# Optimization experiments

Hardware: AMD Instinct MI355X
Metric: run time of the kernel (lower is better)

Reference implementation:

```python
import jax, jax.numpy as jnp
import numpy as np

NEG_SLOPE = 0.2   # LeakyReLU default negative slope (GATv2 + nn.LeakyReLU)
K_NEIGH = 16      # att_args['num_neighs']


def leaky(x):
    return jnp.where(x >= 0, x, NEG_SLOPE * x)


def knn_idx(x_feat, y_feat, k):
    """Per-batch KNN of y in x (feature space). x_feat,y_feat: [B,M,C] -> [B,M,k] local idx into x."""
    d = (jnp.sum(y_feat * y_feat, -1, keepdims=True)
         - 2.0 * jnp.einsum('bmc,bnc->bmn', y_feat, x_feat)
         + jnp.sum(x_feat * x_feat, -1)[:, None, :])   # [B,M,M]
    _, idx = jax.lax.top_k(-d, k)
    return idx


def gatv2_bipartite(x_last, x_past, nbr, Wl, Wr, att_w):
    """Faithful GATv2Conv((last, past), edge_index) with flow='target_to_source',
    heads H, concat=False (mean over heads), bias=False, no self loops.
    x_j = lin_l(x[0]=last) gathered at knn neighbor (col) indices,
    x_i = lin_r(x[1]=past) at query (row) indices; each query has exactly K edges."""
    N, C = x_last.shape
    H = att_w.shape[0]
    xl = (x_last @ Wl).reshape(N, H, C)          # [N,H,C]
    xr = (x_past @ Wr).reshape(N, H, C)          # [N,H,C]
    xlj = xl[nbr]                                 # [N,K,H,C] gathered source msgs
    e = jnp.einsum('nkhc,hc->nkh', leaky(xlj + xr[:, None]), att_w)  # [N,K,H]
    a = jax.nn.softmax(e, axis=1)                 # softmax over each target's K edges
    out = jnp.einsum('nkh,nkhc->nhc', a, xlj)     # [N,H,C]
    return out.mean(axis=1)                       # concat=False -> head mean, [N,C]


def reference(pc_encoded_seq, W1, b1, W2, b2, Wl, Wr, att_w, batch_size, m_points):
    T, N, C = pc_encoded_seq.shape
    B, M = batch_size, m_points
    G = W2.shape[1]
    # node_level_proj (Linear-LeakyReLU-Linear-LeakyReLU) + global_mean_pool per frame
    h = leaky(leaky(pc_encoded_seq @ W1 + b1) @ W2 + b2)      # [T,N,G]
    global_fea = h.reshape(T, B, M, G).mean(axis=2)            # [T,B,G]
    # frame-level ScaledDotProductAttention: q = last frame, k=v = past frames
    q = global_fea[-1][:, None, :]                             # [B,1,G]
    kv = jnp.transpose(global_fea[:-1], (1, 0, 2))             # [B,T-1,G]
    score = jnp.einsum('bqg,btg->bqt', q, kv) / jnp.sqrt(jnp.asarray(G, jnp.float32))
    attn = jax.nn.softmax(score, axis=-1)                      # [B,1,T-1]
    last = pc_encoded_seq[-1]                                  # [N,C]
    lastb = last.reshape(B, M, C)
    offs = (jnp.arange(B) * M)[:, None, None]
    res = []
    for i in range(T - 1):   # small fixed frame count
        past = pc_encoded_seq[i]
        nbr = knn_idx(past.reshape(B, M, C), lastb, K_NEIGH) + offs  # global idx
        out = gatv2_bipartite(last, past, nbr.reshape(N, K_NEIGH), Wl, Wr, att_w)
        res.append(out.reshape(B, M, C))
    res = jnp.stack(res, axis=1)                               # [B,T-1,M,C]
    fw = attn[:, 0, :, None, None]                             # [B,T-1,1,1]
    weighted = jnp.sum(res * fw, axis=1)                       # [B,M,C]
    tm_out = jnp.concatenate([last, weighted.reshape(N, C)], axis=-1)  # [N,2C]
    return tm_out


def setup_inputs() -> dict:
    key = jax.random.key(0)
    ks = jax.random.split(key, 8)
    T, B, M, C, G, H = 5, 4, 4096, 128, 1024, 4
    N = B * M
    s = lambda fan: 1.0 / np.sqrt(fan)
    return {
        'pc_encoded_seq': jax.random.normal(ks[0], (T, N, C), jnp.float32),
        'W1': jax.random.normal(ks[1], (C, 128), jnp.float32) * s(C),
        'b1': jnp.zeros((128,), jnp.float32),
        'W2': jax.random.normal(ks[2], (128, G), jnp.float32) * s(128),
        'b2': jnp.zeros((G,), jnp.float32),
        'Wl': jax.random.normal(ks[3], (C, H * C), jnp.float32) * s(C),
        'Wr': jax.random.normal(ks[4], (C, H * C), jnp.float32) * s(C),
        'att_w': jax.random.normal(ks[5], (H, C), jnp.float32) * s(C),
        'batch_size': B,
        'm_points': M,
    }
```

## Files before the change

### kernel.cpp

```cpp
#include <hip/hip_runtime.h>
#include <hip/hip_bf16.h>
#include <hip/hip_fp16.h>


typedef __bf16 v8bf __attribute__((ext_vector_type(8)));
typedef float  v4f  __attribute__((ext_vector_type(4)));

__device__ __forceinline__ float lrelu(float x) { return fmaxf(x, 0.2f * x); }

__device__ __forceinline__ unsigned short f2bf(float x) {
  __hip_bfloat16 h = __float2bfloat16(x);
  return __builtin_bit_cast(unsigned short, h);
}
__device__ __forceinline__ float bf2f(unsigned short u) {
  unsigned int t = ((unsigned int)u) << 16;
  return __builtin_bit_cast(float, t);
}

__device__ __forceinline__ unsigned fkey(float v) {
  unsigned b = __builtin_bit_cast(unsigned, v);
  return b ^ (((unsigned)((int)b >> 31)) | 0x80000000u);
}
__device__ __forceinline__ float finv(unsigned k) {
  unsigned m = (unsigned)((int)k >> 31);
  unsigned b = k ^ ((~m) | 0x80000000u);
  return __builtin_bit_cast(float, b);
}

#define GLOAD_LDS16(gp, lp)                                                   \
  __builtin_amdgcn_global_load_lds(                                           \
      (const __attribute__((address_space(1))) void*)(gp),                    \
      (__attribute__((address_space(3))) void*)(lp), 16, 0, 0)

#define RBAR() do { __builtin_amdgcn_s_barrier(); asm volatile("" ::: "memory"); } while (0)
#define LWAIT() do { asm volatile("s_waitcnt lgkmcnt(0)" ::: "memory");        \
                     __builtin_amdgcn_sched_barrier(0); } while (0)

template<int EP>
__global__ __launch_bounds__(256, 2)
void nt_mfma(const unsigned short* __restrict__ A, const unsigned short* __restrict__ B,
             const float* __restrict__ aux, void* __restrict__ outv, int K, int ldc)
{
  __shared__ __align__(16) unsigned short smem[3 * 8192];
  const int tid = threadIdx.x;
  const int l = tid & 63;
  const int w = tid >> 6;
  const int wm = w & 1, wn = w >> 1;
  const int m0 = blockIdx.y << 7, n0 = blockIdx.x << 7;
  const int fr = l & 15, quad = l >> 4;
  const int kt = K >> 5;
  const int xq4 = quad ^ ((fr >> 1) & 3);

  const int r0 = tid >> 2;
  const int sw = (tid & 3) ^ ((tid >> 3) & 3);
  const unsigned short* Aa = A + (size_t)(m0 + r0) * K + sw * 8;
  const unsigned short* Ab = Aa + (size_t)64 * K;
  const unsigned short* Ba = B + (size_t)(n0 + r0) * K + sw * 8;
  const unsigned short* Bb = Ba + (size_t)64 * K;

  auto stage = [&](int bi, int ks) {
    unsigned short* As = smem + bi * 8192;
    unsigned short* Bs = As + 4096;
    GLOAD_LDS16(Aa + ks * 32, As + tid * 8);
    GLOAD_LDS16(Ab + ks * 32, As + (tid + 256) * 8);
    GLOAD_LDS16(Ba + ks * 32, Bs + tid * 8);
    GLOAD_LDS16(Bb + ks * 32, Bs + (tid + 256) * 8);
  };

  v4f acc[4][4];
#pragma unroll
  for (int i = 0; i < 4; ++i)
#pragma unroll
    for (int j = 0; j < 4; ++j) acc[i][j] = (v4f){0.f, 0.f, 0.f, 0.f};

  stage(0, 0);
  if (kt > 1) stage(1, 1);
  int cur = 0, pend = (kt > 1) ? 2 : 1, sn = 2;

  for (int ks = 0; ks < kt; ++ks) {
    if (pend == 2) asm volatile("s_waitcnt vmcnt(4)" ::: "memory");
    else           asm volatile("s_waitcnt vmcnt(0)" ::: "memory");
    RBAR();
    int nb = cur + 2; if (nb >= 3) nb -= 3;
    if (sn < kt) { stage(nb, sn); ++sn; } else { --pend; }
    const unsigned short* As = smem + cur * 8192;
    const unsigned short* Bs = As + 4096;
    v8bf af[4], bfr[4];
#pragma unroll
    for (int i = 0; i < 4; ++i)
      af[i] = *(const v8bf*)(As + (wm * 64 + i * 16 + fr) * 32 + xq4 * 8);
#pragma unroll
    for (int j = 0; j < 4; ++j)
      bfr[j] = *(const v8bf*)(Bs + (wn * 64 + j * 16 + fr) * 32 + xq4 * 8);
#pragma unroll
    for (int i = 0; i < 4; ++i)
#pragma unroll
      for (int j = 0; j < 4; ++j)
        acc[i][j] = __builtin_amdgcn_mfma_f32_16x16x32_bf16(af[i], bfr[j], acc[i][j], 0, 0, 0);
    __builtin_amdgcn_sched_barrier(0);
    if (++cur == 3) cur = 0;
  }

  if (EP == 1) {
    unsigned short* O = (unsigned short*)outv;
#pragma unroll
    for (int j = 0; j < 4; ++j) {
      int col = n0 + wn * 64 + j * 16 + fr;
      float bias = aux[col];
#pragma unroll
      for (int i = 0; i < 4; ++i) {
        int row = m0 + wm * 64 + i * 16 + quad * 4;
#pragma unroll
        for (int r = 0; r < 4; ++r)
          O[(size_t)(row + r) * ldc + col] = f2bf(lrelu(acc[i][j][r] + bias));
      }
    }
  } else if (EP == 2) {
    __syncthreads();
    float* red = (float*)smem;
#pragma unroll
    for (int j = 0; j < 4; ++j) {
      int lcol = wn * 64 + j * 16 + fr;
      float bias = aux[n0 + lcol];
      float s = 0.f;
#pragma unroll
      for (int i = 0; i < 4; ++i)
#pragma unroll
        for (int r = 0; r < 4; ++r) s += lrelu(acc[i][j][r] + bias);
      s += __shfl_xor(s, 16);
      s += __shfl_xor(s, 32);
      if (quad == 0) red[w * 128 + lcol] = s;
    }
    __syncthreads();
    if (tid < 128) {
      float s = (tid < 64) ? red[0 * 128 + tid] + red[1 * 128 + tid]
                           : red[2 * 128 + tid] + red[3 * 128 + tid];
      atomicAdd((float*)outv + ((m0 >> 12) << 10) + n0 + tid, s * (1.0f / 4096.0f));
    }
  } else {
    __half* O = (__half*)outv;
#pragma unroll
    for (int j = 0; j < 4; ++j) {
      int col = n0 + wn * 64 + j * 16 + fr;
#pragma unroll
      for (int i = 0; i < 4; ++i) {
        int row = m0 + wm * 64 + i * 16 + quad * 4;
#pragma unroll
        for (int r = 0; r < 4; ++r)
          O[(size_t)(row + r) * ldc + col] = __float2half(acc[i][j][r]);
      }
    }
  }
}

#define TOPN 20
#define FB   10
#define PSTR 11

__global__ __launch_bounds__(256, 4)
void knn_coarse(const unsigned short* __restrict__ seqbf,
                const float* __restrict__ xsq, int* __restrict__ candOut)
{
  __shared__ __align__(16) unsigned short bsm[8192];
  __shared__ unsigned pushK[64 * PSTR];
  __shared__ int      cntW[64];

  const int tid = threadIdx.x;
  const int l = tid & 63;
  const int w = tid >> 6;
  const int blk = blockIdx.x;
  const int pair = ((blk & 7) << 1) | ((blk >> 3) & 1);
  const int rb = blk >> 4;
  const int f = pair >> 2, b = pair & 3;
  const int m0 = rb << 6;
  const int fr = l & 15, quad = l >> 4;
  const int xq4 = quad ^ ((fr >> 1) & 3);

  const unsigned short* ybase = seqbf + ((size_t)65536 + b * 4096) * 128;
  const unsigned short* xbase = seqbf + ((size_t)(f * 16384 + b * 4096)) * 128;
  const float* xq = xsq + f * 16384 + b * 4096;

  const int r0 = tid >> 2;
  const int sw = (tid & 3) ^ ((tid >> 3) & 3);

  v8bf afr[4];
#pragma unroll
  for (int ksp = 0; ksp < 4; ++ksp)
    afr[ksp] = *(const v8bf*)(ybase + (size_t)(m0 + w * 16 + fr) * 128 + ksp * 32 + quad * 8);

  unsigned tk[TOPN];
#pragma unroll
  for (int k = 0; k < TOPN; ++k) tk[k] = 0u;
  float tauReg = -3.0e38f;
  if (l < 16) cntW[w * 16 + l] = 0;
  float tc[4];
#pragma unroll
  for (int r = 0; r < 4; ++r) tc[r] = -3.0e38f;
  LWAIT();

  for (int ct = 0; ct < 32; ++ct) {
    const int n0 = ct << 7;
    const unsigned short* Bt = xbase + (size_t)(n0 + r0) * 128 + sw * 8;

    RBAR();
    GLOAD_LDS16(Bt, bsm + tid * 8);
    GLOAD_LDS16(Bt + 64 * 128, bsm + (tid + 256) * 8);
    GLOAD_LDS16(Bt + 32, bsm + 4096 + tid * 8);
    GLOAD_LDS16(Bt + 64 * 128 + 32, bsm + 4096 + (tid + 256) * 8);
    float xsv[8];
#pragma unroll
    for (int j = 0; j < 8; ++j) xsv[j] = xq[n0 + j * 16 + fr];
    asm volatile("s_waitcnt vmcnt(0)" ::: "memory");
    RBAR();

    v4f acc[8];
#pragma unroll
    for (int j = 0; j < 8; ++j) acc[j] = (v4f){0.f, 0.f, 0.f, 0.f};

#pragma unroll
    for (int ksp = 0; ksp < 2; ++ksp) {
      v8bf bfr[8];
#pragma unroll
      for (int j = 0; j < 8; ++j)
        bfr[j] = *(const v8bf*)(bsm + ksp * 4096 + (j * 16 + fr) * 32 + xq4 * 8);
#pragma unroll
      for (int j = 0; j < 8; ++j)
        acc[j] = __builtin_amdgcn_mfma_f32_16x16x32_bf16(afr[ksp], bfr[j], acc[j], 0, 0, 0);
    }
    LWAIT();
    RBAR();

    GLOAD_LDS16(Bt + 2 * 32, bsm + tid * 8);
    GLOAD_LDS16(Bt + 64 * 128 + 2 * 32, bsm + (tid + 256) * 8);
    GLOAD_LDS16(Bt + 3 * 32, bsm + 4096 + tid * 8);
    GLOAD_LDS16(Bt + 64 * 128 + 3 * 32, bsm + 4096 + (tid + 256) * 8);
    asm volatile("s_waitcnt vmcnt(0)" ::: "memory");
    RBAR();

#pragma unroll
    for (int ksp = 0; ksp < 2; ++ksp) {
      v8bf bfr[8];
#pragma unroll
      for (int j = 0; j < 8; ++j)
        bfr[j] = *(const v8bf*)(bsm + ksp * 4096 + (j * 16 + fr) * 32 + xq4 * 8);
#pragma unroll
      for (int j = 0; j < 8; ++j)
        acc[j] = __builtin_amdgcn_mfma_f32_16x16x32_bf16(afr[2 + ksp], bfr[j], acc[j], 0, 0, 0);
    }

#pragma unroll
    for (int j = 0; j < 8; ++j)
#pragma unroll
      for (int r = 0; r < 4; ++r)
        acc[j][r] = 2.f * acc[j][r] - xsv[j];

    if (ct == 0) {
#pragma unroll
      for (int r = 0; r < 4; ++r) {
        float t1 = fmaxf(acc[0][r], acc[1][r]);
        float t2 = fminf(acc[0][r], acc[1][r]);
#pragma unroll
        for (int j = 2; j < 8; ++j) {
          float v = acc[j][r];
          float hi = fmaxf(t1, v);
          t2 = fmaxf(t2, fminf(t1, v));
          t1 = hi;
        }
#pragma unroll
        for (int off = 1; off <= 8; off <<= 1)
          t2 = fminf(t2, __shfl_xor(t2, off));
        tc[r] = t2;
        float tq = __shfl(t2, (l >> 2) << 4);
        if (l < 16 && (l & 3) == r) tauReg = tq;
      }
    }

    unsigned int pushed = 0u;
    for (;;) {
#pragma unroll
      for (int r = 0; r < 4; ++r) {
        const float tau = tc[r];
        int mca = 0;
#pragma unroll
        for (int j = 0; j < 8; ++j) {
          const int bit = j * 4 + r;
          if (acc[j][r] >= tau && !((pushed >> bit) & 1u)) mca |= (1 << j);
        }
        if (__any(mca != 0)) {
          const int lrow = w * 16 + quad * 4 + r;
#pragma unroll
          for (int j = 0; j < 8; ++j)
            if ((mca >> j) & 1) {
              int pos = atomicAdd(&cntW[lrow], 1);
              if (pos < FB) {
                pushK[lrow * PSTR + pos] =
                    (fkey(acc[j][r]) & 0xFFFFF000u) | (unsigned)(n0 + j * 16 + fr);
                pushed |= (1u << (j * 4 + r));
              }
            }
        }
      }
      LWAIT();
      bool ov = false;
      if (l < 16) {
        const int grow = w * 16 + l;
        int c = cntW[grow];
        int cc = c < FB ? c : FB;
        for (int q = 0; q < cc; ++q) {
          unsigned k = pushK[grow * PSTR + q];
          if (k > tk[TOPN - 1]) {
#pragma unroll
            for (int i = TOPN - 1; i >= 1; --i)
              tk[i] = (k > tk[i - 1]) ? tk[i - 1] : (k > tk[i] ? k : tk[i]);
            tk[0] = (k > tk[0]) ? k : tk[0];
          }
        }
        if (tk[TOPN - 1] != 0u)
          tauReg = fmaxf(tauReg, finv(tk[TOPN - 1] & 0xFFFFF000u));
        ov = c > FB;
        cntW[grow] = 0;
      }
      LWAIT();
#pragma unroll
      for (int r = 0; r < 4; ++r)
        tc[r] = __shfl(tauReg, quad * 4 + r);
      if (!__any(ov)) break;
    }
  }

  if (l < 16) {
    const int grow = w * 16 + l;
    int* outp = candOut + ((size_t)(f * 16384 + b * 4096 + m0 + grow)) * TOPN;
#pragma unroll
    for (int k = 0; k < TOPN; ++k) outp[k] = (int)(tk[k] & 0xFFFu);
  }
}

__global__ __launch_bounds__(256)
void knn_rescore(const float* __restrict__ seq, const float* __restrict__ xsq,
                 const int* __restrict__ cand, int* __restrict__ nbrOut)
{
  __shared__ float sc[4][20];
  const int tid = threadIdx.x;
  const int l = tid & 63;
  const int wq = tid >> 6;
  const int blk = blockIdx.x;
  const int pair = ((blk & 7) << 1) | ((blk >> 3) & 1);
  const int qb = blk >> 4;
  const int f = pair >> 2, b = pair & 3;
  const int qloc = qb * 4 + wq;
  const int gq = pair * 4096 + qloc;

  const int c8 = l & 7;
  const int h  = l >> 3;
  const float* yrow = seq + ((size_t)65536 + b * 4096 + qloc) * 128 + h * 16;
  float4 y0 = *(const float4*)(yrow);
  float4 y1 = *(const float4*)(yrow + 4);
  float4 y2 = *(const float4*)(yrow + 8);
  float4 y3 = *(const float4*)(yrow + 12);
  const float* xslice = seq + (size_t)(f * 16384 + (b << 12)) * 128;
  const float* xsqs = xsq + f * 16384 + (b << 12);
  const int* cq = cand + (size_t)gq * 20;

#pragma unroll
  for (int rd = 0; rd < 3; ++rd) {
    int cr = rd * 8 + c8;
    int crc = cr < 20 ? cr : 0;
    int cj = cq[crc];
    const float* xr = xslice + (size_t)cj * 128 + h * 16;
    float4 x0 = *(const float4*)(xr);
    float4 x1 = *(const float4*)(xr + 4);
    float4 x2 = *(const float4*)(xr + 8);
    float4 x3 = *(const float4*)(xr + 12);
    float p = y0.x * x0.x + y0.y * x0.y + y0.z * x0.z + y0.w * x0.w
            + y1.x * x1.x + y1.y * x1.y + y1.z * x1.z + y1.w * x1.w
            + y2.x * x2.x + y2.y * x2.y + y2.z * x2.z + y2.w * x2.w
            + y3.x * x3.x + y3.y * x3.y + y3.z * x3.z + y3.w * x3.w;
    p += __shfl_xor(p, 8);
    p += __shfl_xor(p, 16);
    p += __shfl_xor(p, 32);
    if (h == 0 && cr < 20) sc[wq][cr] = 2.f * p - xsqs[cj];
  }
  LWAIT();
  if (l < 20) {
    float myv = sc[wq][l];
    int rank = 0;
#pragma unroll
    for (int j = 0; j < 20; ++j) {
      float vj = sc[wq][j];
      rank += (vj > myv || (vj == myv && j < l)) ? 1 : 0;
    }
    if (rank < 16)
      nbrOut[(size_t)gq * 16 + rank] = (b << 12) + cq[l];
  }
}

__global__ __launch_bounds__(256)
void convert_inputs(const float* __restrict__ seq, unsigned short* __restrict__ seqbf,
                    unsigned short* __restrict__ ylay, unsigned short* __restrict__ xlay,
                    float* __restrict__ xsq)
{
  const int tid = threadIdx.x;
  const int row = blockIdx.x * 8 + (tid >> 5);
  const int c4 = tid & 31;
  float4 v = *(const float4*)(seq + (size_t)row * 128 + c4 * 4);
  ushort4 hi, lo;
  hi.x = f2bf(v.x); lo.x = f2bf(v.x - bf2f(hi.x));
  hi.y = f2bf(v.y); lo.y = f2bf(v.y - bf2f(hi.y));
  hi.z = f2bf(v.z); lo.z = f2bf(v.z - bf2f(hi.z));
  hi.w = f2bf(v.w); lo.w = f2bf(v.w - bf2f(hi.w));
  *(ushort4*)(seqbf + (size_t)row * 128 + c4 * 4) = hi;
  float ss = v.x * v.x + v.y * v.y + v.z * v.z + v.w * v.w;
#pragma unroll
  for (int off = 16; off; off >>= 1) ss += __shfl_xor(ss, off);
  if (row < 65536) {
    unsigned short* p = xlay + (size_t)row * 384 + c4 * 4;
    *(ushort4*)(p) = hi; *(ushort4*)(p + 128) = lo; *(ushort4*)(p + 256) = hi;
    if (c4 == 0) xsq[row] = ss;
  } else {
    unsigned short* p = ylay + (size_t)(row - 65536) * 384 + c4 * 4;
    *(ushort4*)(p) = hi; *(ushort4*)(p + 128) = hi; *(ushort4*)(p + 256) = lo;
  }
}

__global__ __launch_bounds__(256)
void convert_weights(const float* __restrict__ W1, const float* __restrict__ W2,
                     const float* __restrict__ Wl, const float* __restrict__ Wr,
                     const float* __restrict__ aw,
                     unsigned short* __restrict__ W1t, unsigned short* __restrict__ W2t,
                     unsigned short* __restrict__ Wlv, unsigned short* __restrict__ Wrv,
                     __half* __restrict__ awh)
{
  int idx = blockIdx.x * 256 + threadIdx.x;
  if (idx < 16384) {
    int n = idx >> 7, k = idx & 127;
    W1t[idx] = f2bf(W1[k * 128 + n]);
  } else if (idx < 147456) {
    int i = idx - 16384; int n = i >> 7, k = i & 127;
    W2t[i] = f2bf(W2[k * 1024 + n]);
  } else if (idx < 344064) {
    int i = idx - 147456; int n = i / 384, k = i % 384;
    int s = k >> 7, kk = k & 127;
    float wv = Wl[kk * 512 + n];
    unsigned short h = f2bf(wv);
    Wlv[i] = (s == 1) ? f2bf(wv - bf2f(h)) : h;
  } else if (idx < 540672) {
    int i = idx - 344064; int n = i / 384, k = i % 384;
    int s = k >> 7, kk = k & 127;
    float wv = Wr[kk * 512 + n];
    unsigned short h = f2bf(wv);
    Wrv[i] = (s == 2) ? f2bf(wv - bf2f(h)) : h;
  } else if (idx < 541184) {
    int i = idx - 540672;
    awh[i] = __float2half(aw[i]);
  }
}

__global__ __launch_bounds__(1024)
void temporal_attn(const float* __restrict__ gfea, float* __restrict__ attnw)
{
  const int tid = threadIdx.x;
  const int w = tid >> 6, l = tid & 63;
  const int b = w >> 2, i = w & 3;
  const float* q  = gfea + (16 + b) * 1024;
  const float* kv = gfea + (i * 4 + b) * 1024;
  float p = 0.f;
  for (int g = l; g < 1024; g += 64) p += q[g] * kv[g];
#pragma unroll
  for (int off = 32; off; off >>= 1) p += __shfl_xor(p, off);
  __shared__ float sc[16];
  if (l == 0) sc[w] = p * 0.03125f;
  __syncthreads();
  if (tid < 4) {
    float v0 = sc[tid * 4 + 0], v1 = sc[tid * 4 + 1];
    float v2 = sc[tid * 4 + 2], v3 = sc[tid * 4 + 3];
    float mm = fmaxf(fmaxf(v0, v1), fmaxf(v2, v3));
    v0 = __expf(v0 - mm); v1 = __expf(v1 - mm);
    v2 = __expf(v2 - mm); v3 = __expf(v3 - mm);
    float inv = 1.f / (v0 + v1 + v2 + v3);
    attnw[tid * 4 + 0] = v0 * inv;
    attnw[tid * 4 + 1] = v1 * inv;
    attnw[tid * 4 + 2] = v2 * inv;
    attnw[tid * 4 + 3] = v3 * inv;
  }
}

__global__ __launch_bounds__(256)
void gat6(const __half* __restrict__ xlh, const __half* __restrict__ xrh,
          const int* __restrict__ nbr, const __half* __restrict__ awh,
          const float* __restrict__ attnw, float* __restrict__ wgt4)
{
  const int tid = threadIdx.x;
  const int l = tid & 63;
  const int blk = blockIdx.x;
  const int r8 = blk & 7;
  const int b = r8 >> 1;
  const int g = ((blk >> 3) << 1) | (r8 & 1);
  const int f = g >> 10;
  const int n4 = g & 1023;
  const int qid = f * 16384 + b * 4096 + n4 * 4 + (tid >> 6);
  const int h = l >> 4, cp = l & 15;
  const float fw = attnw[b * 4 + f] * 0.25f;

  const int jl = nbr[qid * 16 + (l & 15)];
  const __half* xbase = xlh + h * 128 + cp * 8;

  const __half2* xrp = (const __half2*)(xrh + (size_t)qid * 512 + h * 128 + cp * 8);
  float2 xr0 = __half22float2(xrp[0]), xr1 = __half22float2(xrp[1]);
  float2 xr2 = __half22float2(xrp[2]), xr3 = __half22float2(xrp[3]);
  const __half2* awp = (const __half2*)(awh + h * 128 + cp * 8);
  float2 aw0 = __half22float2(awp[0]), aw1 = __half22float2(awp[1]);
  float2 aw2 = __half22float2(awp[2]), aw3 = __half22float2(awp[3]);

  float m = -3.0e38f, s = 0.f;
  float o[8];
#pragma unroll
  for (int c = 0; c < 8; ++c) o[c] = 0.f;

  for (int ch = 0; ch < 2; ++ch) {
    float4 xv[8];
#pragma unroll
    for (int k = 0; k < 8; ++k) {
      int j = __shfl(jl, ch * 8 + k);
      xv[k] = *(const float4*)(xbase + (size_t)j * 512);
    }
    float e[8];
#pragma unroll
    for (int k = 0; k < 8; ++k) {
      const __half2* hp = (const __half2*)&xv[k];
      float2 x0 = __half22float2(hp[0]), x1 = __half22float2(hp[1]);
      float2 x2 = __half22float2(hp[2]), x3 = __half22float2(hp[3]);
      float p = 0.f;
      p += lrelu(x0.x + xr0.x) * aw0.x + lrelu(x0.y + xr0.y) * aw0.y;
      p += lrelu(x1.x + xr1.x) * aw1.x + lrelu(x1.y + xr1.y) * aw1.y;
      p += lrelu(x2.x + xr2.x) * aw2.x + lrelu(x2.y + xr2.y) * aw2.y;
      p += lrelu(x3.x + xr3.x) * aw3.x + lrelu(x3.y + xr3.y) * aw3.y;
      p += __shfl_xor(p, 1);
      p += __shfl_xor(p, 2);
      p += __shfl_xor(p, 4);
      p += __shfl_xor(p, 8);
      e[k] = p;
    }
    float mc = e[0];
#pragma unroll
    for (int k = 1; k < 8; ++k) mc = fmaxf(mc, e[k]);
    float mn = fmaxf(m, mc);
    float cr = __expf(m - mn);
    s *= cr;
#pragma unroll
    for (int c = 0; c < 8; ++c) o[c] *= cr;
#pragma unroll
    for (int k = 0; k < 8; ++k) {
      float a = __expf(e[k] - mn);
      s += a;
      const __half2* hp = (const __half2*)&xv[k];
      float2 f0 = __half22float2(hp[0]);
      float2 f1 = __half22float2(hp[1]);
      float2 f2 = __half22float2(hp[2]);
      float2 f3 = __half22float2(hp[3]);
      o[0] += a * f0.x; o[1] += a * f0.y;
      o[2] += a * f1.x; o[3] += a * f1.y;
      o[4] += a * f2.x; o[5] += a * f2.y;
      o[6] += a * f3.x; o[7] += a * f3.y;
    }
    m = mn;
  }

  const float sc = fw / s;
#pragma unroll
  for (int c = 0; c < 8; ++c) {
    float t = o[c] * sc;
    t += __shfl_xor(t, 16);
    t += __shfl_xor(t, 32);
    o[c] = t;
  }
  if (l < 16) {
    float* wp = wgt4 + (size_t)qid * 128 + l * 8;
    *(float4*)(wp)     = make_float4(o[0], o[1], o[2], o[3]);
    *(float4*)(wp + 4) = make_float4(o[4], o[5], o[6], o[7]);
  }
}

__global__ __launch_bounds__(256)
void finalize2(const float* __restrict__ last, const float* __restrict__ wgt4,
               float* __restrict__ out)
{
  int idx = blockIdx.x * 256 + threadIdx.x;
  int n = idx >> 6, q = idx & 63;
  float4 v;
  if (q < 32) {
    v = *(const float4*)(last + (size_t)n * 128 + 4 * q);
  } else {
    int c = (q - 32) * 4;
    v = make_float4(0.f, 0.f, 0.f, 0.f);
#pragma unroll
    for (int f = 0; f < 4; ++f) {
      float4 t = *(const float4*)(wgt4 + ((size_t)f * 16384 + n) * 128 + c);
      v.x += t.x; v.y += t.y; v.z += t.z; v.w += t.w;
    }
  }
  *(float4*)(out + (size_t)n * 256 + 4 * q) = v;
}

extern "C" void kernel_launch(void* const* d_in, const int* in_sizes, int n_in,
                              void* d_out, int out_size, void* d_ws, size_t ws_size,
                              hipStream_t stream)
{
  (void)in_sizes; (void)n_in; (void)out_size; (void)ws_size;
  const float* seq = (const float*)d_in[0];
  const float* W1  = (const float*)d_in[1];
  const float* b1  = (const float*)d_in[2];
  const float* W2  = (const float*)d_in[3];
  const float* b2  = (const float*)d_in[4];
  const float* Wl  = (const float*)d_in[5];
  const float* Wr  = (const float*)d_in[6];
  const float* aw  = (const float*)d_in[7];
  float* out = (float*)d_out;

  float* ws = (float*)d_ws;
  __half* xrh          = (__half*)ws;
  unsigned short* seqbf = (unsigned short*)(ws + 16777216);
  unsigned short* h1bf  = (unsigned short*)(ws + 22020096);
  int* cand20           = (int*)(ws + 22020096);
  __half* xlh           = (__half*)(ws + 22020096);
  unsigned short* ylay  = (unsigned short*)(ws + 27262976);
  unsigned short* xlay  = (unsigned short*)(ws + 30408704);
  float* wgt4           = ws + 30408704;
  float* gfea           = ws + 42991616;
  float* attn           = gfea + 20480;
  float* xsq            = attn + 16;
  int*   nbr            = (int*)(xsq + 65536);
  unsigned short* W1t   = (unsigned short*)(nbr + 1048576);
  unsigned short* W2t   = W1t + 16384;
  unsigned short* Wlv   = W2t + 131072;
  unsigned short* Wrv   = Wlv + 196608;
  __half* awh           = (__half*)(Wrv + 196608);

  (void)hipMemsetAsync(gfea, 0, 20480 * sizeof(float), stream);

  convert_inputs<<<10240, 256, 0, stream>>>(seq, seqbf, ylay, xlay, xsq);
  convert_weights<<<2114, 256, 0, stream>>>(W1, W2, Wl, Wr, aw, W1t, W2t, Wlv, Wrv, awh);

  nt_mfma<1><<<dim3(1, 640), 256, 0, stream>>>(seqbf, W1t, b1, h1bf, 128, 128);
  nt_mfma<2><<<dim3(8, 640), 256, 0, stream>>>(h1bf, W2t, b2, gfea, 128, 0);
  temporal_attn<<<1, 1024, 0, stream>>>(gfea, attn);

  knn_coarse<<<1024, 256, 0, stream>>>(seqbf, xsq, cand20);
  knn_rescore<<<16384, 256, 0, stream>>>(seq, xsq, cand20, nbr);

  nt_mfma<3><<<dim3(4, 128), 256, 0, stream>>>(ylay, Wlv, nullptr, xlh, 384, 512);
  nt_mfma<3><<<dim3(4, 512), 256, 0, stream>>>(xlay, Wrv, nullptr, xrh, 384, 512);

  gat6<<<16384, 256, 0, stream>>>(xlh, xrh, nbr, awh, attn, wgt4);

  finalize2<<<4096, 256, 0, stream>>>(seq + (size_t)4 * 16384 * 128, wgt4, out);
}
```

Measured before the change: 769.8 us.

## Split KNN coarse search across candidate halves and merge partial top-20 lists

The coarse KNN kernel now splits the 4096 candidate columns into two halves handled by separate blocks, doubling the grid. Each block writes its full top-20 keys, and a new merge kernel combines the two sorted lists into the final 20 candidate indices. Occupancy hints rise to 8 blocks per SM. The push loop gains a cheap per-row max pre-check that skips the per-element scan and the LDS round trip when no value beats the threshold. The cost is an extra kernel launch and intermediate key traffic, and each half starts with a weaker threshold, so more candidates get pushed.

```diff
diff --git a/kernel.cpp b/kernel.cpp
--- a/kernel.cpp
+++ b/kernel.cpp
@@ -157,9 +157,9 @@
 #define FB   10
 #define PSTR 11
 
-__global__ __launch_bounds__(256, 4)
+__global__ __launch_bounds__(256, 8)
 void knn_coarse(const unsigned short* __restrict__ seqbf,
-                const float* __restrict__ xsq, int* __restrict__ candOut)
+                const float* __restrict__ xsq, unsigned* __restrict__ ckeys)
 {
   __shared__ __align__(16) unsigned short bsm[8192];
   __shared__ unsigned pushK[64 * PSTR];
@@ -170,7 +170,8 @@
   const int w = tid >> 6;
   const int blk = blockIdx.x;
   const int pair = ((blk & 7) << 1) | ((blk >> 3) & 1);
-  const int rb = blk >> 4;
+  const int h = (blk >> 4) & 1;
+  const int rb = blk >> 5;
   const int f = pair >> 2, b = pair & 3;
   const int m0 = rb << 6;
   const int fr = l & 15, quad = l >> 4;
@@ -198,8 +199,8 @@
   for (int r = 0; r < 4; ++r) tc[r] = -3.0e38f;
   LWAIT();
 
-  for (int ct = 0; ct < 32; ++ct) {
-    const int n0 = ct << 7;
+  for (int ct = 0; ct < 16; ++ct) {
+    const int n0 = (h << 11) + (ct << 7);
     const unsigned short* Bt = xbase + (size_t)(n0 + r0) * 128 + sw * 8;
 
     RBAR();
@@ -277,29 +278,44 @@
 
     unsigned int pushed = 0u;
     for (;;) {
+      bool didPush = false;
+      int hit = 0;
 #pragma unroll
       for (int r = 0; r < 4; ++r) {
-        const float tau = tc[r];
-        int mca = 0;
-#pragma unroll
-        for (int j = 0; j < 8; ++j) {
-          const int bit = j * 4 + r;
-          if (acc[j][r] >= tau && !((pushed >> bit) & 1u)) mca |= (1 << j);
-        }
-        if (__any(mca != 0)) {
-          const int lrow = w * 16 + quad * 4 + r;
-#pragma unroll
-          for (int j = 0; j < 8; ++j)
-            if ((mca >> j) & 1) {
-              int pos = atomicAdd(&cntW[lrow], 1);
-              if (pos < FB) {
-                pushK[lrow * PSTR + pos] =
-                    (fkey(acc[j][r]) & 0xFFFFF000u) | (unsigned)(n0 + j * 16 + fr);
-                pushed |= (1u << (j * 4 + r));
-              }
+        float m = acc[0][r];
+#pragma unroll
+        for (int j = 1; j < 8; ++j) m = fmaxf(m, acc[j][r]);
+        if (m >= tc[r]) hit |= 1 << r;
+      }
+      if (__any(hit != 0)) {
+#pragma unroll
+        for (int r = 0; r < 4; ++r) {
+          if (__any(hit & (1 << r))) {
+            const float tau = tc[r];
+            int mca = 0;
+#pragma unroll
+            for (int j = 0; j < 8; ++j) {
+              const int bit = j * 4 + r;
+              if (acc[j][r] >= tau && !((pushed >> bit) & 1u)) mca |= (1 << j);
             }
+            if (__any(mca != 0)) {
+              const int lrow = w * 16 + quad * 4 + r;
+#pragma unroll
+              for (int j = 0; j < 8; ++j)
+                if ((mca >> j) & 1) {
+                  int pos = atomicAdd(&cntW[lrow], 1);
+                  if (pos < FB) {
+                    pushK[lrow * PSTR + pos] =
+                        (fkey(acc[j][r]) & 0xFFFFF000u) | (unsigned)(n0 + j * 16 + fr);
+                    pushed |= (1u << (j * 4 + r));
+                    didPush = true;
+                  }
+                }
+            }
+          }
         }
       }
+      if (!__any(didPush)) break;
       LWAIT();
       bool ov = false;
       if (l < 16) {
@@ -330,9 +346,33 @@
 
   if (l < 16) {
     const int grow = w * 16 + l;
-    int* outp = candOut + ((size_t)(f * 16384 + b * 4096 + m0 + grow)) * TOPN;
-#pragma unroll
-    for (int k = 0; k < TOPN; ++k) outp[k] = (int)(tk[k] & 0xFFFu);
+    unsigned* outp = ckeys + ((size_t)(f * 16384 + b * 4096 + m0 + grow)) * 40 + h * 20;
+#pragma unroll
+    for (int k = 0; k < TOPN; ++k) outp[k] = tk[k];
+  }
+}
+
+__global__ __launch_bounds__(256)
+void knn_merge(const unsigned* __restrict__ ckeys, int* __restrict__ cand20)
+{
+  __shared__ unsigned lbuf[256 * 40];
+  const int tid = threadIdx.x;
+  const size_t base = (size_t)blockIdx.x * 10240;
+#pragma unroll
+  for (int i = 0; i < 40; ++i)
+    lbuf[tid + i * 256] = ckeys[base + tid + i * 256];
+  LWAIT();
+  __syncthreads();
+  const unsigned* A = lbuf + tid * 40;
+  int ia = 0, ib = 20;
+  unsigned ka = A[0], kb = A[20];
+  int* outp = cand20 + ((size_t)blockIdx.x * 256 + tid) * 20;
+#pragma unroll
+  for (int k = 0; k < 20; ++k) {
+    bool ta = ka >= kb;
+    outp[k] = (int)((ta ? ka : kb) & 0xFFFu);
+    if (ta) { ++ia; ka = (ia < 20) ? A[ia] : 0u; }
+    else    { ++ib; kb = (ib < 40) ? A[ib] : 0u; }
   }
 }
 
@@ -621,7 +661,8 @@
   __half* xrh          = (__half*)ws;
   unsigned short* seqbf = (unsigned short*)(ws + 16777216);
   unsigned short* h1bf  = (unsigned short*)(ws + 22020096);
-  int* cand20           = (int*)(ws + 22020096);
+  unsigned* ckeys       = (unsigned*)(ws + 22020096);
+  int* cand20           = (int*)(ws + 22020096 + 2621440);
   __half* xlh           = (__half*)(ws + 22020096);
   unsigned short* ylay  = (unsigned short*)(ws + 27262976);
   unsigned short* xlay  = (unsigned short*)(ws + 30408704);
@@ -645,7 +686,8 @@
   nt_mfma<2><<<dim3(8, 640), 256, 0, stream>>>(h1bf, W2t, b2, gfea, 128, 0);
   temporal_attn<<<1, 1024, 0, stream>>>(gfea, attn);
 
-  knn_coarse<<<1024, 256, 0, stream>>>(seqbf, xsq, cand20);
+  knn_coarse<<<2048, 256, 0, stream>>>(seqbf, xsq, ckeys);
+  knn_merge<<<256, 256, 0, stream>>>(ckeys, cand20);
   knn_rescore<<<16384, 256, 0, stream>>>(seq, xsq, cand20, nbr);
 
   nt_mfma<3><<<dim3(4, 128), 256, 0, stream>>>(ylay, Wlv, nullptr, xlh, 384, 512);
```

Result: slower. 1.665 ms (+116.2%).

## Drop split-bf16 compensation in GAT projections and prefilter KNN push loop

Applied to the files above, without the earlier changes.

The GAT lin_l/lin_r projections previously used a three-term hi/lo bf16 split (K=384) to emulate fp32 accuracy. They now use plain bf16 inputs and weights with K=128, reading directly from the existing seqbf buffer, which removes the xlay/ylay staging writes and two-thirds of the GEMM work. The KNN coarse push loop also adds a cheap per-row max check, skips rows with no candidates above threshold, and exits early when nothing was pushed. The precision reduction risks larger numerical error in attention scores and outputs.

```diff
diff --git a/kernel.cpp b/kernel.cpp
--- a/kernel.cpp
+++ b/kernel.cpp
@@ -277,29 +277,44 @@
 
     unsigned int pushed = 0u;
     for (;;) {
+      bool didPush = false;
+      int hit = 0;
 #pragma unroll
       for (int r = 0; r < 4; ++r) {
-        const float tau = tc[r];
-        int mca = 0;
-#pragma unroll
-        for (int j = 0; j < 8; ++j) {
-          const int bit = j * 4 + r;
-          if (acc[j][r] >= tau && !((pushed >> bit) & 1u)) mca |= (1 << j);
-        }
-        if (__any(mca != 0)) {
-          const int lrow = w * 16 + quad * 4 + r;
-#pragma unroll
-          for (int j = 0; j < 8; ++j)
-            if ((mca >> j) & 1) {
-              int pos = atomicAdd(&cntW[lrow], 1);
-              if (pos < FB) {
-                pushK[lrow * PSTR + pos] =
-                    (fkey(acc[j][r]) & 0xFFFFF000u) | (unsigned)(n0 + j * 16 + fr);
-                pushed |= (1u << (j * 4 + r));
-              }
+        float m = acc[0][r];
+#pragma unroll
+        for (int j = 1; j < 8; ++j) m = fmaxf(m, acc[j][r]);
+        if (m >= tc[r]) hit |= 1 << r;
+      }
+      if (__any(hit != 0)) {
+#pragma unroll
+        for (int r = 0; r < 4; ++r) {
+          if (__any(hit & (1 << r))) {
+            const float tau = tc[r];
+            int mca = 0;
+#pragma unroll
+            for (int j = 0; j < 8; ++j) {
+              const int bit = j * 4 + r;
+              if (acc[j][r] >= tau && !((pushed >> bit) & 1u)) mca |= (1 << j);
             }
+            if (__any(mca != 0)) {
+              const int lrow = w * 16 + quad * 4 + r;
+#pragma unroll
+              for (int j = 0; j < 8; ++j)
+                if ((mca >> j) & 1) {
+                  int pos = atomicAdd(&cntW[lrow], 1);
+                  if (pos < FB) {
+                    pushK[lrow * PSTR + pos] =
+                        (fkey(acc[j][r]) & 0xFFFFF000u) | (unsigned)(n0 + j * 16 + fr);
+                    pushed |= (1u << (j * 4 + r));
+                    didPush = true;
+                  }
+                }
+            }
+          }
         }
       }
+      if (!__any(didPush)) break;
       LWAIT();
       bool ov = false;
       if (l < 16) {
@@ -397,29 +412,20 @@
 
 __global__ __launch_bounds__(256)
 void convert_inputs(const float* __restrict__ seq, unsigned short* __restrict__ seqbf,
-                    unsigned short* __restrict__ ylay, unsigned short* __restrict__ xlay,
                     float* __restrict__ xsq)
 {
   const int tid = threadIdx.x;
   const int row = blockIdx.x * 8 + (tid >> 5);
   const int c4 = tid & 31;
   float4 v = *(const float4*)(seq + (size_t)row * 128 + c4 * 4);
-  ushort4 hi, lo;
-  hi.x = f2bf(v.x); lo.x = f2bf(v.x - bf2f(hi.x));
-  hi.y = f2bf(v.y); lo.y = f2bf(v.y - bf2f(hi.y));
-  hi.z = f2bf(v.z); lo.z = f2bf(v.z - bf2f(hi.z));
-  hi.w = f2bf(v.w); lo.w = f2bf(v.w - bf2f(hi.w));
+  ushort4 hi;
+  hi.x = f2bf(v.x); hi.y = f2bf(v.y); hi.z = f2bf(v.z); hi.w = f2bf(v.w);
   *(ushort4*)(seqbf + (size_t)row * 128 + c4 * 4) = hi;
-  float ss = v.x * v.x + v.y * v.y + v.z * v.z + v.w * v.w;
-#pragma unroll
-  for (int off = 16; off; off >>= 1) ss += __shfl_xor(ss, off);
   if (row < 65536) {
-    unsigned short* p = xlay + (size_t)row * 384 + c4 * 4;
-    *(ushort4*)(p) = hi; *(ushort4*)(p + 128) = lo; *(ushort4*)(p + 256) = hi;
+    float ss = v.x * v.x + v.y * v.y + v.z * v.z + v.w * v.w;
+#pragma unroll
+    for (int off = 16; off; off >>= 1) ss += __shfl_xor(ss, off);
     if (c4 == 0) xsq[row] = ss;
-  } else {
-    unsigned short* p = ylay + (size_t)(row - 65536) * 384 + c4 * 4;
-    *(ushort4*)(p) = hi; *(ushort4*)(p + 128) = hi; *(ushort4*)(p + 256) = lo;
   }
 }
 
@@ -438,20 +444,14 @@
   } else if (idx < 147456) {
     int i = idx - 16384; int n = i >> 7, k = i & 127;
     W2t[i] = f2bf(W2[k * 1024 + n]);
-  } else if (idx < 344064) {
-    int i = idx - 147456; int n = i / 384, k = i % 384;
-    int s = k >> 7, kk = k & 127;
-    float wv = Wl[kk * 512 + n];
-    unsigned short h = f2bf(wv);
-    Wlv[i] = (s == 1) ? f2bf(wv - bf2f(h)) : h;
-  } else if (idx < 540672) {
-    int i = idx - 344064; int n = i / 384, k = i % 384;
-    int s = k >> 7, kk = k & 127;
-    float wv = Wr[kk * 512 + n];
-    unsigned short h = f2bf(wv);
-    Wrv[i] = (s == 2) ? f2bf(wv - bf2f(h)) : h;
-  } else if (idx < 541184) {
-    int i = idx - 540672;
+  } else if (idx < 212992) {
+    int i = idx - 147456; int n = i >> 7, k = i & 127;
+    Wlv[i] = f2bf(Wl[k * 512 + n]);
+  } else if (idx < 278528) {
+    int i = idx - 212992; int n = i >> 7, k = i & 127;
+    Wrv[i] = f2bf(Wr[k * 512 + n]);
+  } else if (idx < 279040) {
+    int i = idx - 278528;
     awh[i] = __float2half(aw[i]);
   }
 }
@@ -623,8 +623,6 @@
   unsigned short* h1bf  = (unsigned short*)(ws + 22020096);
   int* cand20           = (int*)(ws + 22020096);
   __half* xlh           = (__half*)(ws + 22020096);
-  unsigned short* ylay  = (unsigned short*)(ws + 27262976);
-  unsigned short* xlay  = (unsigned short*)(ws + 30408704);
   float* wgt4           = ws + 30408704;
   float* gfea           = ws + 42991616;
   float* attn           = gfea + 20480;
@@ -633,13 +631,13 @@
   unsigned short* W1t   = (unsigned short*)(nbr + 1048576);
   unsigned short* W2t   = W1t + 16384;
   unsigned short* Wlv   = W2t + 131072;
-  unsigned short* Wrv   = Wlv + 196608;
-  __half* awh           = (__half*)(Wrv + 196608);
+  unsigned short* Wrv   = Wlv + 65536;
+  __half* awh           = (__half*)(Wrv + 65536);
 
   (void)hipMemsetAsync(gfea, 0, 20480 * sizeof(float), stream);
 
-  convert_inputs<<<10240, 256, 0, stream>>>(seq, seqbf, ylay, xlay, xsq);
-  convert_weights<<<2114, 256, 0, stream>>>(W1, W2, Wl, Wr, aw, W1t, W2t, Wlv, Wrv, awh);
+  convert_inputs<<<10240, 256, 0, stream>>>(seq, seqbf, xsq);
+  convert_weights<<<1090, 256, 0, stream>>>(W1, W2, Wl, Wr, aw, W1t, W2t, Wlv, Wrv, awh);
 
   nt_mfma<1><<<dim3(1, 640), 256, 0, stream>>>(seqbf, W1t, b1, h1bf, 128, 128);
   nt_mfma<2><<<dim3(8, 640), 256, 0, stream>>>(h1bf, W2t, b2, gfea, 128, 0);
@@ -648,8 +646,8 @@
   knn_coarse<<<1024, 256, 0, stream>>>(seqbf, xsq, cand20);
   knn_rescore<<<16384, 256, 0, stream>>>(seq, xsq, cand20, nbr);
 
-  nt_mfma<3><<<dim3(4, 128), 256, 0, stream>>>(ylay, Wlv, nullptr, xlh, 384, 512);
-  nt_mfma<3><<<dim3(4, 512), 256, 0, stream>>>(xlay, Wrv, nullptr, xrh, 384, 512);
+  nt_mfma<3><<<dim3(4, 128), 256, 0, stream>>>(seqbf + (size_t)65536 * 128, Wlv, nullptr, xlh, 128, 512);
+  nt_mfma<3><<<dim3(4, 512), 256, 0, stream>>>(seqbf, Wrv, nullptr, xrh, 128, 512);
 
   gat6<<<16384, 256, 0, stream>>>(xlh, xrh, nbr, awh, attn, wgt4);
 
```

After: 755.0 us. Within noise of the previous version (-1.9%).
